# Performance work log

Hardware: AMD Instinct MI355X
Metric: run time of the kernel (lower is better)

## Reference

```python
import jax, jax.numpy as jnp
import numpy as np

BATCH, FIELD0, EMB = 1024, 32, 64
LAYER_SIZES = (128, 128, 128)  # split_half=True -> hidden field sizes [32, 64, 64]


def setup_inputs() -> dict:
    key = jax.random.key(0)
    ks = jax.random.split(key, 7)
    x = jax.random.normal(ks[0], (BATCH, FIELD0, EMB), dtype=jnp.float32)
    # Conv1D(kernel_size=1) weights: (in_channels=f0*fi, filters=layer_size), plus bias.
    field_sizes = [FIELD0]
    params = {}
    for i, size in enumerate(LAYER_SIZES):
        fi = field_sizes[-1]
        fan_in = FIELD0 * fi
        scale = 1.0 / np.sqrt(fan_in)
        params[f"W{i}"] = jax.random.normal(ks[1 + 2 * i], (fan_in, size), dtype=jnp.float32) * scale
        params[f"b{i}"] = jnp.zeros((size,), dtype=jnp.float32)
        field_sizes.append(size // 2 if i != len(LAYER_SIZES) - 1 else size)
    return {"x": x, **params}


def reference(x, W0, b0, W1, b1, W2, b2):
    # CIN: outer product + 1x1 conv (a matmul over the flattened field-pair axis)
    # fused as a single bilinear contraction per layer:
    #   cur[b,k,e] = sum_{i,j} x[b,i,e] * hidden[b,j,e] * W[i,j,k] + b[k]
    Ws = [(W0, b0), (W1, b1), (W2, b2)]
    f0 = x.shape[1]
    hidden = x
    final_outputs = []
    n_layers = len(Ws)
    for idx, (W, b) in enumerate(Ws):
        fi = hidden.shape[1]
        Wr = W.reshape(f0, fi, W.shape[-1])  # channel m = i*fi + j (row-major reshape)
        cur = jnp.einsum('bie,bje,ijk->bke', x, hidden, Wr) + b[None, :, None]
        # activation=None -> linear
        if idx != n_layers - 1:
            half = cur.shape[1] // 2
            hidden, direct = cur[:, :half, :], cur[:, half:, :]
        else:
            direct = cur
        final_outputs.append(direct)
    result = jnp.concatenate(final_outputs, axis=1)  # (B, 64+64+128, E)
    return jnp.sum(result, axis=-1)  # (B, 256)
```

## Files before the change

kernel.cpp:

```cpp
#include <hip/hip_runtime.h>
#include <hip/hip_bf16.h>
#include <cstdint>


typedef _Float16 half8  __attribute__((ext_vector_type(8)));
typedef _Float16 half4_ __attribute__((ext_vector_type(4)));
typedef _Float16 half2_ __attribute__((ext_vector_type(2)));
typedef float    f32x4  __attribute__((ext_vector_type(4)));

__global__ void pack_w_all(const float* __restrict__ W0, _Float16* __restrict__ Wt0,
                           const float* __restrict__ W1, _Float16* __restrict__ Wt1,
                           const float* __restrict__ W2, _Float16* __restrict__ Wt2)
{
    __shared__ _Float16 ldsT[128 * 33];
    const int blk = blockIdx.x, t = threadIdx.x;
    const float* W;
    _Float16* Wt;
    int c;
    if (blk < 32)       { W = W0; Wt = Wt0; c = blk; }
    else if (blk < 96)  { W = W1; Wt = Wt1; c = blk - 32; }
    else                { W = W2; Wt = Wt2; c = blk - 96; }

    for (int p = t; p < 32 * 128; p += 256) {
        int kk = p >> 7, m = p & 127;
        ldsT[m * 33 + kk] = (_Float16)W[(size_t)(c * 32 + kk) * 128 + m];
    }
    __syncthreads();
    int m = t >> 1, kk0 = (t & 1) * 16;
    half8 v0, v1;
#pragma unroll
    for (int i = 0; i < 8; ++i) {
        v0[i] = ldsT[m * 33 + kk0 + i];
        v1[i] = ldsT[m * 33 + kk0 + 8 + i];
    }
    *(half8*)(Wt + (size_t)c * 4096 + t * 16)     = v0;
    *(half8*)(Wt + (size_t)c * 4096 + t * 16 + 8) = v1;
}

__global__ __launch_bounds__(256, 3)
void cin_fused(const float* __restrict__ x,
               const _Float16* __restrict__ Wt0,
               const _Float16* __restrict__ Wt1,
               const float* __restrict__ bs0,
               const float* __restrict__ bs1,
               _Float16* __restrict__ S0,
               _Float16* __restrict__ S1,
               _Float16* __restrict__ S2)
{
    __shared__ alignas(16) char smem[45056];
    _Float16* slotA = (_Float16*)smem;
    _Float16* slotB = (_Float16*)(smem + 18432);
    _Float16* sX    = (_Float16*)(smem + 36864);

    const int t = threadIdx.x, lane = t & 63, w = t >> 6;
    const int ks = w & 1, bb = w >> 1;
    const int lr = lane & 15, q = lane >> 4;
    const int b0 = blockIdx.x * 2;
    const int batch = b0 + bb;

    {
        const float4* xv = (const float4*)(x + (size_t)b0 * 2048);
#pragma unroll
        for (int s = 0; s < 4; ++s) {
            int p4 = t + s * 256;
            float4 v = xv[p4];
            int bb2 = p4 >> 9, idx = (p4 & 511) * 4;
            int i = idx >> 6, e0 = idx & 63;
            _Float16 h0 = (_Float16)v.x, h1 = (_Float16)v.y;
            _Float16 h2 = (_Float16)v.z, h3 = (_Float16)v.w;
            half4_ pk = {h0, h1, h2, h3};
            *(half4_*)(sX + bb2 * 2048 + i * 64 + e0) = pk;
            _Float16* hb = slotA + bb2 * 2560;
            hb[(e0 + 0) * 40 + i] = h0;
            hb[(e0 + 1) * 40 + i] = h1;
            hb[(e0 + 2) * 40 + i] = h2;
            hb[(e0 + 3) * 40 + i] = h3;
        }
    }
    __syncthreads();

    f32x4 acc[4][4];

    auto kloop = [&](const _Float16* WtL, int cBeg, int cEnd, int ish,
                     const _Float16* hbase, int ph) {
#pragma unroll
        for (int mt = 0; mt < 4; ++mt)
#pragma unroll
            for (int nt = 0; nt < 4; ++nt)
                acc[mt][nt] = f32x4{0.0f, 0.0f, 0.0f, 0.0f};
        const _Float16* aG = WtL + lr * 32 + q * 8;
        const _Float16* hP = hbase + bb * (ph << 6) + lr * ph + q * 8;
        const _Float16* xP = sX + bb * 2048 + lr;
        half8 afA[4], afB[4], hvA[4], hvB[4];
        _Float16 xsA[4], xsB[4];
        auto pf = [&](half8* af, half8* hv, _Float16* xs, int c) {
            const int i  = c >> ish;
            const int j0 = (c - (i << ish)) << 5;
            const _Float16* ag = aG + (size_t)c * 4096;
#pragma unroll
            for (int mt = 0; mt < 4; ++mt) af[mt] = *(const half8*)(ag + mt * 512);
#pragma unroll
            for (int nt = 0; nt < 4; ++nt) {
                hv[nt] = *(const half8*)(hP + nt * (ph << 4) + j0);
                xs[nt] = xP[(i << 6) + (nt << 4)];
            }
        };
        auto cp = [&](half8* af, half8* hv, _Float16* xs) {
#pragma unroll
            for (int nt = 0; nt < 4; ++nt) {
                half2_ xv2 = {xs[nt], xs[nt]};
                half8 xv8 = __builtin_shufflevector(xv2, xv2, 0, 1, 0, 1, 0, 1, 0, 1);
                half8 bf = hv[nt] * xv8;
#pragma unroll
                for (int mt = 0; mt < 4; ++mt)
                    acc[mt][nt] = __builtin_amdgcn_mfma_f32_16x16x32_f16(
                        af[mt], bf, acc[mt][nt], 0, 0, 0);
            }
        };
        pf(afA, hvA, xsA, cBeg);
        for (int c = cBeg; c < cEnd; c += 2) {
            pf(afB, hvB, xsB, c + 1);
            cp(afA, hvA, xsA);
            if (c + 2 < cEnd) pf(afA, hvA, xsA, c + 2);
            cp(afB, hvB, xsB);
        }
    };

    auto sgemm = [&](const _Float16* hJ, int jp, int fi, _Float16* Sdst) {
        const _Float16* axp = sX + bb * 2048 + (ks * 16 + lr) * 64 + q * 8;
        const int njt = fi >> 4;
        for (int jt = 0; jt < njt; ++jt) {
            f32x4 sa = {0.0f, 0.0f, 0.0f, 0.0f};
#pragma unroll
            for (int c2 = 0; c2 < 2; ++c2) {
                half8 a = *(const half8*)(axp + c2 * 32);
                half8 b = *(const half8*)(hJ + (jt * 16 + lr) * jp + q * 8 + c2 * 32);
                sa = __builtin_amdgcn_mfma_f32_16x16x32_f16(a, b, sa, 0, 0, 0);
            }
#pragma unroll
            for (int r = 0; r < 4; ++r)
                Sdst[(size_t)batch * (32 * fi) + (ks * 16 + q * 4 + r) * fi
                     + jt * 16 + lr] = (_Float16)sa[r];
        }
    };

    auto partial_out = [&](_Float16* slot) {
#pragma unroll
        for (int mt = 0; mt < 4; ++mt)
#pragma unroll
            for (int nt = 0; nt < 4; ++nt) {
                int e = nt * 16 + lr;
                int j = mt * 16 + q * 4;
                half4_ pv;
#pragma unroll
                for (int r = 0; r < 4; ++r) pv[r] = (_Float16)acc[mt][nt][r];
                *(half4_*)(slot + bb * 4608 + e * 72 + j) = pv;
            }
    };

    sgemm(sX + bb * 2048, 64, 32, S0);
    kloop(Wt0, ks * 16, ks * 16 + 16, 0, slotA, 40);
    if (ks == 1) partial_out(slotB);
    __syncthreads();
    if (ks == 0) {
#pragma unroll
        for (int mt = 0; mt < 4; ++mt)
#pragma unroll
            for (int nt = 0; nt < 4; ++nt) {
                int e = nt * 16 + lr;
                int j = mt * 16 + q * 4;
                half4_ pv = *(const half4_*)(slotB + bb * 4608 + e * 72 + j);
                half4_ vh;
#pragma unroll
                for (int r = 0; r < 4; ++r) {
                    float v = acc[mt][nt][r] + (float)pv[r] + bs0[j + r];
                    vh[r] = (_Float16)v;
                    slotA[bb * 4608 + (j + r) * 72 + e] = (_Float16)v;
                }
                *(half4_*)(slotB + bb * 4608 + e * 72 + j) = vh;
            }
    }
    __syncthreads();

    sgemm(slotA + bb * 4608, 72, 64, S1);
    kloop(Wt1, ks * 32, ks * 32 + 32, 1, slotB, 72);
    __syncthreads();
    if (ks == 1) partial_out(slotB);
    __syncthreads();
    if (ks == 0) {
#pragma unroll
        for (int mt = 0; mt < 4; ++mt)
#pragma unroll
            for (int nt = 0; nt < 4; ++nt) {
                int e = nt * 16 + lr;
                int j = mt * 16 + q * 4;
                half4_ pv = *(const half4_*)(slotB + bb * 4608 + e * 72 + j);
#pragma unroll
                for (int r = 0; r < 4; ++r)
                    slotA[bb * 4608 + (j + r) * 72 + e]
                        = (_Float16)(acc[mt][nt][r] + (float)pv[r] + bs1[j + r]);
            }
    }
    __syncthreads();

    sgemm(slotA + bb * 4608, 72, 64, S2);
}

__global__ __launch_bounds__(256, 4)
void cin_direct(const _Float16* __restrict__ S0v, const _Float16* __restrict__ S1v,
                const _Float16* __restrict__ S2v,
                const _Float16* __restrict__ Wt0, const _Float16* __restrict__ Wt1,
                const _Float16* __restrict__ Wt2,
                const float* __restrict__ bs0, const float* __restrict__ bs1,
                const float* __restrict__ bs2,
                float* __restrict__ out)
{
    const int t = threadIdx.x, lane = t & 63;
    const int lr = lane & 15, q = lane >> 4;
    const int W = blockIdx.x * 4 + (t >> 6);

    const _Float16 *S, *Wt;
    const float* bias;
    int fan, nch, dm0, ob, idx;
    if (W < 256)      { S = S0v; Wt = Wt0; bias = bs0; fan = 1024; nch = 32; dm0 = 64; ob = 0;   idx = W; }
    else if (W < 512) { S = S1v; Wt = Wt1; bias = bs1; fan = 2048; nch = 64; dm0 = 64; ob = 64;  idx = W - 256; }
    else              { S = S2v; Wt = Wt2; bias = bs2; fan = 2048; nch = 64; dm0 = 0;  ob = 128; idx = W - 512; }
    const int bt = idx & 63, kt = idx >> 6;
    const int bbase = bt * 16;

    const _Float16* aG = Wt + (dm0 + kt * 16 + lr) * 32 + q * 8;
    const _Float16* bG = S + (size_t)(bbase + lr) * fan + q * 8;

    f32x4 acc = {0.0f, 0.0f, 0.0f, 0.0f};
    half8 aA = *(const half8*)(aG);
    half8 bA = *(const half8*)(bG);
    for (int c = 0; c < nch; c += 2) {
        half8 aB = *(const half8*)(aG + (size_t)(c + 1) * 4096);
        half8 bB = *(const half8*)(bG + (c + 1) * 32);
        acc = __builtin_amdgcn_mfma_f32_16x16x32_f16(aA, bA, acc, 0, 0, 0);
        if (c + 2 < nch) {
            aA = *(const half8*)(aG + (size_t)(c + 2) * 4096);
            bA = *(const half8*)(bG + (c + 2) * 32);
        }
        acc = __builtin_amdgcn_mfma_f32_16x16x32_f16(aB, bB, acc, 0, 0, 0);
    }
#pragma unroll
    for (int r = 0; r < 4; ++r) {
        int kl = kt * 16 + q * 4 + r;
        out[(size_t)(bbase + lr) * 256 + ob + kl] = acc[r] + 64.0f * bias[dm0 + kl];
    }
}

extern "C" void kernel_launch(void* const* d_in, const int* in_sizes, int n_in,
                              void* d_out, int out_size, void* d_ws, size_t ws_size,
                              hipStream_t stream)
{
    const float* x  = (const float*)d_in[0];
    const float* W0 = (const float*)d_in[1];
    const float* b0 = (const float*)d_in[2];
    const float* W1 = (const float*)d_in[3];
    const float* b1 = (const float*)d_in[4];
    const float* W2 = (const float*)d_in[5];
    const float* b2 = (const float*)d_in[6];
    float* out = (float*)d_out;

    char* ws = (char*)d_ws;
    _Float16* Wt0 = (_Float16*)(ws + 0);
    _Float16* Wt1 = (_Float16*)(ws + 262144);
    _Float16* Wt2 = (_Float16*)(ws + 786432);
    _Float16* S0  = (_Float16*)(ws + 1310720);
    _Float16* S1  = (_Float16*)(ws + 3407872);
    _Float16* S2  = (_Float16*)(ws + 7602176);
    (void)in_sizes; (void)n_in; (void)out_size; (void)ws_size;

    hipLaunchKernelGGL(pack_w_all, dim3(160), dim3(256), 0, stream,
                       W0, Wt0, W1, Wt1, W2, Wt2);

    hipLaunchKernelGGL(cin_fused, dim3(512), dim3(256), 0, stream,
                       x, Wt0, Wt1, b0, b1, S0, S1, S2);

    hipLaunchKernelGGL(cin_direct, dim3(256), dim3(256), 0, stream,
                       S0, S1, S2, Wt0, Wt1, Wt2, b0, b1, b2, out);
}
```

Before: 122.3 us.

## Fuse pack, CIN, and direct-projection kernels into one persistent kernel with grid barriers

```diff
diff --git a/kernel.cpp b/kernel.cpp
--- a/kernel.cpp
+++ b/kernel.cpp
@@ -8,246 +8,270 @@
 typedef _Float16 half2_ __attribute__((ext_vector_type(2)));
 typedef float    f32x4  __attribute__((ext_vector_type(4)));
 
-__global__ void pack_w_all(const float* __restrict__ W0, _Float16* __restrict__ Wt0,
-                           const float* __restrict__ W1, _Float16* __restrict__ Wt1,
-                           const float* __restrict__ W2, _Float16* __restrict__ Wt2)
-{
-    __shared__ _Float16 ldsT[128 * 33];
-    const int blk = blockIdx.x, t = threadIdx.x;
-    const float* W;
-    _Float16* Wt;
-    int c;
-    if (blk < 32)       { W = W0; Wt = Wt0; c = blk; }
-    else if (blk < 96)  { W = W1; Wt = Wt1; c = blk - 32; }
-    else                { W = W2; Wt = Wt2; c = blk - 96; }
-
-    for (int p = t; p < 32 * 128; p += 256) {
-        int kk = p >> 7, m = p & 127;
-        ldsT[m * 33 + kk] = (_Float16)W[(size_t)(c * 32 + kk) * 128 + m];
+__device__ __forceinline__ void grid_bar(unsigned* cnt, unsigned target) {
+    __syncthreads();
+    if (threadIdx.x == 0) {
+        __threadfence();
+        atomicAdd(cnt, 1u);
+        while (__hip_atomic_load(cnt, __ATOMIC_ACQUIRE,
+                                 __HIP_MEMORY_SCOPE_AGENT) < target)
+            __builtin_amdgcn_s_sleep(8);
+        __threadfence();
     }
     __syncthreads();
-    int m = t >> 1, kk0 = (t & 1) * 16;
-    half8 v0, v1;
-#pragma unroll
-    for (int i = 0; i < 8; ++i) {
-        v0[i] = ldsT[m * 33 + kk0 + i];
-        v1[i] = ldsT[m * 33 + kk0 + 8 + i];
-    }
-    *(half8*)(Wt + (size_t)c * 4096 + t * 16)     = v0;
-    *(half8*)(Wt + (size_t)c * 4096 + t * 16 + 8) = v1;
 }
 
 __global__ __launch_bounds__(256, 3)
-void cin_fused(const float* __restrict__ x,
-               const _Float16* __restrict__ Wt0,
-               const _Float16* __restrict__ Wt1,
-               const float* __restrict__ bs0,
-               const float* __restrict__ bs1,
-               _Float16* __restrict__ S0,
-               _Float16* __restrict__ S1,
-               _Float16* __restrict__ S2)
+void cin_all(const float* __restrict__ x,
+             const float* __restrict__ W0, const float* __restrict__ W1,
+             const float* __restrict__ W2,
+             const float* __restrict__ bs0, const float* __restrict__ bs1,
+             const float* __restrict__ bs2,
+             _Float16* __restrict__ Wt0, _Float16* __restrict__ Wt1,
+             _Float16* __restrict__ Wt2,
+             _Float16* __restrict__ S0, _Float16* __restrict__ S1,
+             _Float16* __restrict__ S2,
+             unsigned* __restrict__ bar,
+             float* __restrict__ out)
 {
     __shared__ alignas(16) char smem[45056];
-    _Float16* slotA = (_Float16*)smem;
-    _Float16* slotB = (_Float16*)(smem + 18432);
-    _Float16* sX    = (_Float16*)(smem + 36864);
-
-    const int t = threadIdx.x, lane = t & 63, w = t >> 6;
-    const int ks = w & 1, bb = w >> 1;
-    const int lr = lane & 15, q = lane >> 4;
-    const int b0 = blockIdx.x * 2;
-    const int batch = b0 + bb;
+    const unsigned nblk = gridDim.x;
 
     {
-        const float4* xv = (const float4*)(x + (size_t)b0 * 2048);
-#pragma unroll
-        for (int s = 0; s < 4; ++s) {
-            int p4 = t + s * 256;
-            float4 v = xv[p4];
-            int bb2 = p4 >> 9, idx = (p4 & 511) * 4;
-            int i = idx >> 6, e0 = idx & 63;
-            _Float16 h0 = (_Float16)v.x, h1 = (_Float16)v.y;
-            _Float16 h2 = (_Float16)v.z, h3 = (_Float16)v.w;
-            half4_ pk = {h0, h1, h2, h3};
-            *(half4_*)(sX + bb2 * 2048 + i * 64 + e0) = pk;
-            _Float16* hb = slotA + bb2 * 2560;
-            hb[(e0 + 0) * 40 + i] = h0;
-            hb[(e0 + 1) * 40 + i] = h1;
-            hb[(e0 + 2) * 40 + i] = h2;
-            hb[(e0 + 3) * 40 + i] = h3;
+        const int blk = blockIdx.x, t = threadIdx.x;
+        if (blk < 160) {
+            _Float16* ldsT = (_Float16*)smem;
+            const float* W;
+            _Float16* Wt;
+            int c;
+            if (blk < 32)       { W = W0; Wt = Wt0; c = blk; }
+            else if (blk < 96)  { W = W1; Wt = Wt1; c = blk - 32; }
+            else                { W = W2; Wt = Wt2; c = blk - 96; }
+
+            for (int p = t; p < 32 * 128; p += 256) {
+                int kk = p >> 7, m = p & 127;
+                ldsT[m * 33 + kk] = (_Float16)W[(size_t)(c * 32 + kk) * 128 + m];
+            }
+            __syncthreads();
+            int m = t >> 1, kk0 = (t & 1) * 16;
+            half8 v0, v1;
+#pragma unroll
+            for (int i = 0; i < 8; ++i) {
+                v0[i] = ldsT[m * 33 + kk0 + i];
+                v1[i] = ldsT[m * 33 + kk0 + 8 + i];
+            }
+            *(half8*)(Wt + (size_t)c * 4096 + t * 16)     = v0;
+            *(half8*)(Wt + (size_t)c * 4096 + t * 16 + 8) = v1;
         }
     }
-    __syncthreads();
-
-    f32x4 acc[4][4];
-
-    auto kloop = [&](const _Float16* WtL, int cBeg, int cEnd, int ish,
-                     const _Float16* hbase, int ph) {
-#pragma unroll
-        for (int mt = 0; mt < 4; ++mt)
-#pragma unroll
-            for (int nt = 0; nt < 4; ++nt)
-                acc[mt][nt] = f32x4{0.0f, 0.0f, 0.0f, 0.0f};
-        const _Float16* aG = WtL + lr * 32 + q * 8;
-        const _Float16* hP = hbase + bb * (ph << 6) + lr * ph + q * 8;
-        const _Float16* xP = sX + bb * 2048 + lr;
-        half8 afA[4], afB[4], hvA[4], hvB[4];
-        _Float16 xsA[4], xsB[4];
-        auto pf = [&](half8* af, half8* hv, _Float16* xs, int c) {
-            const int i  = c >> ish;
-            const int j0 = (c - (i << ish)) << 5;
-            const _Float16* ag = aG + (size_t)c * 4096;
-#pragma unroll
-            for (int mt = 0; mt < 4; ++mt) af[mt] = *(const half8*)(ag + mt * 512);
-#pragma unroll
-            for (int nt = 0; nt < 4; ++nt) {
-                hv[nt] = *(const half8*)(hP + nt * (ph << 4) + j0);
-                xs[nt] = xP[(i << 6) + (nt << 4)];
+    grid_bar(bar + 0, nblk);
+
+    {
+        _Float16* slotA = (_Float16*)smem;
+        _Float16* slotB = (_Float16*)(smem + 18432);
+        _Float16* sX    = (_Float16*)(smem + 36864);
+
+        const int t = threadIdx.x, lane = t & 63, w = t >> 6;
+        const int ks = w & 1, bb = w >> 1;
+        const int lr = lane & 15, q = lane >> 4;
+        const int b0 = blockIdx.x * 2;
+        const int batch = b0 + bb;
+
+        {
+            const float4* xv = (const float4*)(x + (size_t)b0 * 2048);
+#pragma unroll
+            for (int s = 0; s < 4; ++s) {
+                int p4 = t + s * 256;
+                float4 v = xv[p4];
+                int bb2 = p4 >> 9, idx = (p4 & 511) * 4;
+                int i = idx >> 6, e0 = idx & 63;
+                _Float16 h0 = (_Float16)v.x, h1 = (_Float16)v.y;
+                _Float16 h2 = (_Float16)v.z, h3 = (_Float16)v.w;
+                half4_ pk = {h0, h1, h2, h3};
+                *(half4_*)(sX + bb2 * 2048 + i * 64 + e0) = pk;
+                _Float16* hb = slotA + bb2 * 2560;
+                hb[(e0 + 0) * 40 + i] = h0;
+                hb[(e0 + 1) * 40 + i] = h1;
+                hb[(e0 + 2) * 40 + i] = h2;
+                hb[(e0 + 3) * 40 + i] = h3;
+            }
+        }
+        __syncthreads();
+
+        f32x4 acc[4][4];
+
+        auto kloop = [&](const _Float16* WtL, int cBeg, int cEnd, int ish,
+                         const _Float16* hbase, int ph) {
+#pragma unroll
+            for (int mt = 0; mt < 4; ++mt)
+#pragma unroll
+                for (int nt = 0; nt < 4; ++nt)
+                    acc[mt][nt] = f32x4{0.0f, 0.0f, 0.0f, 0.0f};
+            const _Float16* aG = WtL + lr * 32 + q * 8;
+            const _Float16* hP = hbase + bb * (ph << 6) + lr * ph + q * 8;
+            const _Float16* xP = sX + bb * 2048 + lr;
+            half8 afA[4], afB[4], hvA[4], hvB[4];
+            _Float16 xsA[4], xsB[4];
+            auto pf = [&](half8* af, half8* hv, _Float16* xs, int c) {
+                const int i  = c >> ish;
+                const int j0 = (c - (i << ish)) << 5;
+                const _Float16* ag = aG + (size_t)c * 4096;
+#pragma unroll
+                for (int mt = 0; mt < 4; ++mt) af[mt] = *(const half8*)(ag + mt * 512);
+#pragma unroll
+                for (int nt = 0; nt < 4; ++nt) {
+                    hv[nt] = *(const half8*)(hP + nt * (ph << 4) + j0);
+                    xs[nt] = xP[(i << 6) + (nt << 4)];
+                }
+            };
+            auto cp = [&](half8* af, half8* hv, _Float16* xs) {
+#pragma unroll
+                for (int nt = 0; nt < 4; ++nt) {
+                    half2_ xv2 = {xs[nt], xs[nt]};
+                    half8 xv8 = __builtin_shufflevector(xv2, xv2, 0, 1, 0, 1, 0, 1, 0, 1);
+                    half8 bf = hv[nt] * xv8;
+#pragma unroll
+                    for (int mt = 0; mt < 4; ++mt)
+                        acc[mt][nt] = __builtin_amdgcn_mfma_f32_16x16x32_f16(
+                            af[mt], bf, acc[mt][nt], 0, 0, 0);
+                }
+            };
+            pf(afA, hvA, xsA, cBeg);
+            for (int c = cBeg; c < cEnd; c += 2) {
+                pf(afB, hvB, xsB, c + 1);
+                cp(afA, hvA, xsA);
+                if (c + 2 < cEnd) pf(afA, hvA, xsA, c + 2);
+                cp(afB, hvB, xsB);
             }
         };
-        auto cp = [&](half8* af, half8* hv, _Float16* xs) {
-#pragma unroll
-            for (int nt = 0; nt < 4; ++nt) {
-                half2_ xv2 = {xs[nt], xs[nt]};
-                half8 xv8 = __builtin_shufflevector(xv2, xv2, 0, 1, 0, 1, 0, 1, 0, 1);
-                half8 bf = hv[nt] * xv8;
-#pragma unroll
-                for (int mt = 0; mt < 4; ++mt)
-                    acc[mt][nt] = __builtin_amdgcn_mfma_f32_16x16x32_f16(
-                        af[mt], bf, acc[mt][nt], 0, 0, 0);
+
+        auto sgemm = [&](const _Float16* hJ, int jp, int fi, _Float16* Sdst) {
+            const _Float16* axp = sX + bb * 2048 + (ks * 16 + lr) * 64 + q * 8;
+            const int njt = fi >> 4;
+            for (int jt = 0; jt < njt; ++jt) {
+                f32x4 sa = {0.0f, 0.0f, 0.0f, 0.0f};
+#pragma unroll
+                for (int c2 = 0; c2 < 2; ++c2) {
+                    half8 a = *(const half8*)(axp + c2 * 32);
+                    half8 b = *(const half8*)(hJ + (jt * 16 + lr) * jp + q * 8 + c2 * 32);
+                    sa = __builtin_amdgcn_mfma_f32_16x16x32_f16(a, b, sa, 0, 0, 0);
+                }
+#pragma unroll
+                for (int r = 0; r < 4; ++r)
+                    Sdst[(size_t)batch * (32 * fi) + (ks * 16 + q * 4 + r) * fi
+                         + jt * 16 + lr] = (_Float16)sa[r];
             }
         };
-        pf(afA, hvA, xsA, cBeg);
-        for (int c = cBeg; c < cEnd; c += 2) {
-            pf(afB, hvB, xsB, c + 1);
-            cp(afA, hvA, xsA);
-            if (c + 2 < cEnd) pf(afA, hvA, xsA, c + 2);
-            cp(afB, hvB, xsB);
-        }
-    };
-
-    auto sgemm = [&](const _Float16* hJ, int jp, int fi, _Float16* Sdst) {
-        const _Float16* axp = sX + bb * 2048 + (ks * 16 + lr) * 64 + q * 8;
-        const int njt = fi >> 4;
-        for (int jt = 0; jt < njt; ++jt) {
-            f32x4 sa = {0.0f, 0.0f, 0.0f, 0.0f};
-#pragma unroll
-            for (int c2 = 0; c2 < 2; ++c2) {
-                half8 a = *(const half8*)(axp + c2 * 32);
-                half8 b = *(const half8*)(hJ + (jt * 16 + lr) * jp + q * 8 + c2 * 32);
-                sa = __builtin_amdgcn_mfma_f32_16x16x32_f16(a, b, sa, 0, 0, 0);
-            }
-#pragma unroll
-            for (int r = 0; r < 4; ++r)
-                Sdst[(size_t)batch * (32 * fi) + (ks * 16 + q * 4 + r) * fi
-                     + jt * 16 + lr] = (_Float16)sa[r];
-        }
-    };
-
-    auto partial_out = [&](_Float16* slot) {
-#pragma unroll
-        for (int mt = 0; mt < 4; ++mt)
-#pragma unroll
-            for (int nt = 0; nt < 4; ++nt) {
-                int e = nt * 16 + lr;
-                int j = mt * 16 + q * 4;
-                half4_ pv;
-#pragma unroll
-                for (int r = 0; r < 4; ++r) pv[r] = (_Float16)acc[mt][nt][r];
-                *(half4_*)(slot + bb * 4608 + e * 72 + j) = pv;
-            }
-    };
-
-    sgemm(sX + bb * 2048, 64, 32, S0);
-    kloop(Wt0, ks * 16, ks * 16 + 16, 0, slotA, 40);
-    if (ks == 1) partial_out(slotB);
-    __syncthreads();
-    if (ks == 0) {
-#pragma unroll
-        for (int mt = 0; mt < 4; ++mt)
-#pragma unroll
-            for (int nt = 0; nt < 4; ++nt) {
-                int e = nt * 16 + lr;
-                int j = mt * 16 + q * 4;
-                half4_ pv = *(const half4_*)(slotB + bb * 4608 + e * 72 + j);
-                half4_ vh;
-#pragma unroll
-                for (int r = 0; r < 4; ++r) {
-                    float v = acc[mt][nt][r] + (float)pv[r] + bs0[j + r];
-                    vh[r] = (_Float16)v;
-                    slotA[bb * 4608 + (j + r) * 72 + e] = (_Float16)v;
-                }
-                *(half4_*)(slotB + bb * 4608 + e * 72 + j) = vh;
-            }
+
+        auto partial_out = [&](_Float16* slot) {
+#pragma unroll
+            for (int mt = 0; mt < 4; ++mt)
+#pragma unroll
+                for (int nt = 0; nt < 4; ++nt) {
+                    int e = nt * 16 + lr;
+                    int j = mt * 16 + q * 4;
+                    half4_ pv;
+#pragma unroll
+                    for (int r = 0; r < 4; ++r) pv[r] = (_Float16)acc[mt][nt][r];
+                    *(half4_*)(slot + bb * 4608 + e * 72 + j) = pv;
+                }
+        };
+
+        sgemm(sX + bb * 2048, 64, 32, S0);
+        kloop(Wt0, ks * 16, ks * 16 + 16, 0, slotA, 40);
+        if (ks == 1) partial_out(slotB);
+        __syncthreads();
+        if (ks == 0) {
+#pragma unroll
+            for (int mt = 0; mt < 4; ++mt)
+#pragma unroll
+                for (int nt = 0; nt < 4; ++nt) {
+                    int e = nt * 16 + lr;
+                    int j = mt * 16 + q * 4;
+                    half4_ pv = *(const half4_*)(slotB + bb * 4608 + e * 72 + j);
+                    half4_ vh;
+#pragma unroll
+                    for (int r = 0; r < 4; ++r) {
+                        float v = acc[mt][nt][r] + (float)pv[r] + bs0[j + r];
+                        vh[r] = (_Float16)v;
+                        slotA[bb * 4608 + (j + r) * 72 + e] = (_Float16)v;
+                    }
+                    *(half4_*)(slotB + bb * 4608 + e * 72 + j) = vh;
+                }
+        }
+        __syncthreads();
+
+        sgemm(slotA + bb * 4608, 72, 64, S1);
+        kloop(Wt1, ks * 32, ks * 32 + 32, 1, slotB, 72);
+        __syncthreads();
+        if (ks == 1) partial_out(slotB);
+        __syncthreads();
+        if (ks == 0) {
+#pragma unroll
+            for (int mt = 0; mt < 4; ++mt)
+#pragma unroll
+                for (int nt = 0; nt < 4; ++nt) {
+                    int e = nt * 16 + lr;
+                    int j = mt * 16 + q * 4;
+                    half4_ pv = *(const half4_*)(slotB + bb * 4608 + e * 72 + j);
+#pragma unroll
+                    for (int r = 0; r < 4; ++r)
+                        slotA[bb * 4608 + (j + r) * 72 + e]
+                            = (_Float16)(acc[mt][nt][r] + (float)pv[r] + bs1[j + r]);
+                }
+        }
+        __syncthreads();
+
+        sgemm(slotA + bb * 4608, 72, 64, S2);
     }
-    __syncthreads();
-
-    sgemm(slotA + bb * 4608, 72, 64, S1);
-    kloop(Wt1, ks * 32, ks * 32 + 32, 1, slotB, 72);
-    __syncthreads();
-    if (ks == 1) partial_out(slotB);
-    __syncthreads();
-    if (ks == 0) {
-#pragma unroll
-        for (int mt = 0; mt < 4; ++mt)
-#pragma unroll
-            for (int nt = 0; nt < 4; ++nt) {
-                int e = nt * 16 + lr;
-                int j = mt * 16 + q * 4;
-                half4_ pv = *(const half4_*)(slotB + bb * 4608 + e * 72 + j);
-#pragma unroll
-                for (int r = 0; r < 4; ++r)
-                    slotA[bb * 4608 + (j + r) * 72 + e]
-                        = (_Float16)(acc[mt][nt][r] + (float)pv[r] + bs1[j + r]);
-            }
-    }
-    __syncthreads();
-
-    sgemm(slotA + bb * 4608, 72, 64, S2);
-}
-
-__global__ __launch_bounds__(256, 4)
-void cin_direct(const _Float16* __restrict__ S0v, const _Float16* __restrict__ S1v,
-                const _Float16* __restrict__ S2v,
-                const _Float16* __restrict__ Wt0, const _Float16* __restrict__ Wt1,
-                const _Float16* __restrict__ Wt2,
-                const float* __restrict__ bs0, const float* __restrict__ bs1,
-                const float* __restrict__ bs2,
-                float* __restrict__ out)
-{
-    const int t = threadIdx.x, lane = t & 63;
-    const int lr = lane & 15, q = lane >> 4;
-    const int W = blockIdx.x * 4 + (t >> 6);
-
-    const _Float16 *S, *Wt;
-    const float* bias;
-    int fan, nch, dm0, ob, idx;
-    if (W < 256)      { S = S0v; Wt = Wt0; bias = bs0; fan = 1024; nch = 32; dm0 = 64; ob = 0;   idx = W; }
-    else if (W < 512) { S = S1v; Wt = Wt1; bias = bs1; fan = 2048; nch = 64; dm0 = 64; ob = 64;  idx = W - 256; }
-    else              { S = S2v; Wt = Wt2; bias = bs2; fan = 2048; nch = 64; dm0 = 0;  ob = 128; idx = W - 512; }
-    const int bt = idx & 63, kt = idx >> 6;
-    const int bbase = bt * 16;
-
-    const _Float16* aG = Wt + (dm0 + kt * 16 + lr) * 32 + q * 8;
-    const _Float16* bG = S + (size_t)(bbase + lr) * fan + q * 8;
-
-    f32x4 acc = {0.0f, 0.0f, 0.0f, 0.0f};
-    half8 aA = *(const half8*)(aG);
-    half8 bA = *(const half8*)(bG);
-    for (int c = 0; c < nch; c += 2) {
-        half8 aB = *(const half8*)(aG + (size_t)(c + 1) * 4096);
-        half8 bB = *(const half8*)(bG + (c + 1) * 32);
-        acc = __builtin_amdgcn_mfma_f32_16x16x32_f16(aA, bA, acc, 0, 0, 0);
-        if (c + 2 < nch) {
-            aA = *(const half8*)(aG + (size_t)(c + 2) * 4096);
-            bA = *(const half8*)(bG + (c + 2) * 32);
-        }
-        acc = __builtin_amdgcn_mfma_f32_16x16x32_f16(aB, bB, acc, 0, 0, 0);
-    }
-#pragma unroll
-    for (int r = 0; r < 4; ++r) {
-        int kl = kt * 16 + q * 4 + r;
-        out[(size_t)(bbase + lr) * 256 + ob + kl] = acc[r] + 64.0f * bias[dm0 + kl];
+    grid_bar(bar + 1, nblk);
+
+    {
+        const int t = threadIdx.x, lane = t & 63, w = t >> 6;
+        const int tl = w >> 1, ks = w & 1;
+        const int id = blockIdx.x * 2 + tl;
+        const int lr = lane & 15, q = lane >> 4;
+        const _Float16 *S, *Wt;
+        const float* bias;
+        int fan, nch, dm0, ob, idx;
+        if (id < 256)      { S = S0; Wt = Wt0; bias = bs0; fan = 1024; nch = 32; dm0 = 64; ob = 0;   idx = id; }
+        else if (id < 512) { S = S1; Wt = Wt1; bias = bs1; fan = 2048; nch = 64; dm0 = 64; ob = 64;  idx = id - 256; }
+        else               { S = S2; Wt = Wt2; bias = bs2; fan = 2048; nch = 64; dm0 = 0;  ob = 128; idx = id - 512; }
+        const int bt = idx & 63, kt = idx >> 6;
+        const int bbase = bt * 16;
+        const int hc = nch >> 1, c0 = ks * hc;
+
+        const _Float16* aG = Wt + (dm0 + kt * 16 + lr) * 32 + q * 8;
+        const _Float16* bG = S + (size_t)(bbase + lr) * fan + q * 8;
+
+        f32x4 da = {0.0f, 0.0f, 0.0f, 0.0f};
+        half8 aA = *(const half8*)(aG + (size_t)c0 * 4096);
+        half8 bA = *(const half8*)(bG + c0 * 32);
+        for (int c = c0; c < c0 + hc; c += 2) {
+            half8 aB = *(const half8*)(aG + (size_t)(c + 1) * 4096);
+            half8 bB = *(const half8*)(bG + (c + 1) * 32);
+            da = __builtin_amdgcn_mfma_f32_16x16x32_f16(aA, bA, da, 0, 0, 0);
+            if (c + 2 < c0 + hc) {
+                aA = *(const half8*)(aG + (size_t)(c + 2) * 4096);
+                bA = *(const half8*)(bG + (c + 2) * 32);
+            }
+            da = __builtin_amdgcn_mfma_f32_16x16x32_f16(aB, bB, da, 0, 0, 0);
+        }
+
+        float* dbuf = (float*)smem;
+        if (ks == 1)
+            *(f32x4*)(dbuf + (tl * 64 + lane) * 4) = da;
+        __syncthreads();
+        if (ks == 0) {
+            f32x4 o = *(const f32x4*)(dbuf + (tl * 64 + lane) * 4);
+            da += o;
+#pragma unroll
+            for (int r = 0; r < 4; ++r) {
+                int kl = kt * 16 + q * 4 + r;
+                out[(size_t)(bbase + lr) * 256 + ob + kl]
+                    = da[r] + 64.0f * bias[dm0 + kl];
+            }
+        }
     }
 }
 
@@ -271,14 +295,12 @@
     _Float16* S0  = (_Float16*)(ws + 1310720);
     _Float16* S1  = (_Float16*)(ws + 3407872);
     _Float16* S2  = (_Float16*)(ws + 7602176);
+    unsigned* bar = (unsigned*)(ws + 11796480);
     (void)in_sizes; (void)n_in; (void)out_size; (void)ws_size;
 
-    hipLaunchKernelGGL(pack_w_all, dim3(160), dim3(256), 0, stream,
-                       W0, Wt0, W1, Wt1, W2, Wt2);
-
-    hipLaunchKernelGGL(cin_fused, dim3(512), dim3(256), 0, stream,
-                       x, Wt0, Wt1, b0, b1, S0, S1, S2);
-
-    hipLaunchKernelGGL(cin_direct, dim3(256), dim3(256), 0, stream,
-                       S0, S1, S2, Wt0, Wt1, Wt2, b0, b1, b2, out);
+    hipMemsetAsync(bar, 0, 2 * sizeof(unsigned), stream);
+
+    hipLaunchKernelGGL(cin_all, dim3(512), dim3(256), 0, stream,
+                       x, W0, W1, W2, b0, b1, b2,
+                       Wt0, Wt1, Wt2, S0, S1, S2, bar, out);
 }
```

Result: slower. 260.7 us (+113.3%).
